# Kernel tuning notes

Hardware: AMD Instinct MI355X
Metric: run time of the kernel (lower is better)

The kernel has to match this reference:

```python
import jax, jax.numpy as jnp
import numpy as np

B, N, H = 16, 1024, 1024


def setup_inputs() -> dict:
    key = jax.random.key(0)
    ks = jax.random.split(key, 12)
    inv = 1.0 / np.sqrt(H)
    inp = {
        "x": jax.random.normal(ks[0], (B, N, H), jnp.float32),
        "atom_graph": jax.random.normal(ks[1], (B, N, N), jnp.float32),
        "variable_graph": jax.random.normal(ks[2], (B, N, N), jnp.float32),
        "Wq": jax.random.uniform(ks[3], (H, H), jnp.float32, -inv, inv),
        "bq": jax.random.uniform(ks[4], (H,), jnp.float32, -inv, inv),
        "Wk": jax.random.uniform(ks[5], (H, H), jnp.float32, -inv, inv),
        "bk": jax.random.uniform(ks[6], (H,), jnp.float32, -inv, inv),
        "Wv": jax.random.uniform(ks[7], (H, H), jnp.float32, -inv, inv),
        "bv": jax.random.uniform(ks[8], (H,), jnp.float32, -inv, inv),
        "predicate_pos": jax.random.randint(ks[9], (B, N), 0, 2, jnp.int32),
        "variable_tags": jax.random.randint(ks[10], (B, N), 0, 4, jnp.int32),
    }
    return inp


def _path_pool(h, predicate_pos):
    # h: [B,N,H]; predicate_pos: [B,N] in {0,1}
    b, n, d = h.shape
    i = jnp.arange(n)
    # pos[i-2] (value irrelevant for i<2, those branches handled explicitly)
    pp2 = jnp.pad(predicate_pos, ((0, 0), (2, 0)))[:, :n]  # [B,N]
    # window [s, e): i==0 -> [0,2); i==1 -> [0,3); pos[i-2]==1 -> [i,i+2); else [i-1,i+2)
    s = jnp.where(i < 2, 0, jnp.where(pp2 == 1, i, i - 1))  # [B,N]
    e = jnp.where(i == 0, 2, jnp.where(i == 1, 3, i + 2))    # [N]
    e = jnp.minimum(e, n)
    e = jnp.broadcast_to(e, (b, n))
    # prefix sums along node dim with a leading zero row -> windowed means via gather
    cs = jnp.concatenate([jnp.zeros((b, 1, d), h.dtype), jnp.cumsum(h, axis=1)], axis=1)  # [B,N+1,H]
    win_sum = (jnp.take_along_axis(cs, e[:, :, None], axis=1)
               - jnp.take_along_axis(cs, s[:, :, None], axis=1))  # [B,N,H]
    means = win_sum / (e - s)[:, :, None].astype(h.dtype)
    mask = (predicate_pos == 1).astype(h.dtype)  # [B,N]
    item = (means * mask[:, :, None]).sum(axis=1) / mask.sum(axis=1)[:, None]  # [B,H]
    return jnp.broadcast_to(item[:, None, :], (b, n, d))


def reference(x, atom_graph, variable_graph, Wq, bq, Wk, bk, Wv, bv,
              predicate_pos, variable_tags):
    scale = x.shape[-1] ** (-0.5)
    q = (x @ Wq.T + bq) * scale
    k = x @ Wk.T + bk
    v = x @ Wv.T + bv
    att = jnp.einsum("bnh,bmh->bnm", q, k) + atom_graph + variable_graph
    att = jax.nn.softmax(att, axis=-1)  # dropout is identity in eval
    h = jnp.einsum("bnm,bmh->bnh", att, v)
    return _path_pool(h, predicate_pos)
```

## Files before the change

kernel.cpp:

```cpp
#include <hip/hip_runtime.h>
#include <hip/hip_bf16.h>

#define BATCH 16
#define SEQ   1024
#define DIM   1024

typedef __attribute__((ext_vector_type(8))) short bf16x8;
typedef __attribute__((ext_vector_type(4))) float f32x4;
typedef __attribute__((ext_vector_type(4))) unsigned short us4;

__device__ __forceinline__ float bfu2f(unsigned short u) {
  union { unsigned int i; float f; } c; c.i = ((unsigned int)u) << 16; return c.f;
}
__device__ __forceinline__ unsigned short f2bfu(float f) {
  union { float f; unsigned int i; } c; c.f = f;
  return (unsigned short)((c.i + 0x7FFFu + ((c.i >> 16) & 1u)) >> 16);
}
__device__ __forceinline__ void async16(void* lds, const void* g) {
  __builtin_amdgcn_global_load_lds(
      (const __attribute__((address_space(1))) unsigned int*)g,
      (__attribute__((address_space(3))) unsigned int*)lds, 16, 0, 0);
}

__global__ void cast_xw_kernel(const float* __restrict__ x, const float* __restrict__ Wv,
                               unsigned short* __restrict__ xb,
                               unsigned short* __restrict__ Wvb, int x4) {
  int i = blockIdx.x * blockDim.x + threadIdx.x;
  const float* in; unsigned short* out; int j;
  if (i < x4) { in = x; out = xb; j = i; }
  else { in = Wv; out = Wvb; j = i - x4; }
  f32x4 v = ((const f32x4*)in)[j];
  us4 o;
  o[0] = f2bfu(v[0]); o[1] = f2bfu(v[1]); o[2] = f2bfu(v[2]); o[3] = f2bfu(v[3]);
  ((us4*)out)[j] = o;
}

__global__ void castT_kernel(const float* __restrict__ Wq, const float* __restrict__ Wk,
                             unsigned short* __restrict__ WqT,
                             unsigned short* __restrict__ WkT) {
  const float* in = (blockIdx.z == 0) ? Wq : Wk;
  unsigned short* out = (blockIdx.z == 0) ? WqT : WkT;
  __shared__ float t[64][65];
  const int h0 = blockIdx.x * 64, i0 = blockIdx.y * 64;
  const int tid = threadIdx.x;
  const int sub = tid >> 4, c4 = tid & 15;
#pragma unroll
  for (int p = 0; p < 4; ++p) {
    const int row = p * 16 + sub;
    f32x4 v = *(const f32x4*)(in + (size_t)(h0 + row) * DIM + i0 + c4 * 4);
    t[row][c4 * 4 + 0] = v[0]; t[row][c4 * 4 + 1] = v[1];
    t[row][c4 * 4 + 2] = v[2]; t[row][c4 * 4 + 3] = v[3];
  }
  __syncthreads();
#pragma unroll
  for (int p = 0; p < 4; ++p) {
    const int orow = p * 16 + sub;
    us4 o;
    o[0] = f2bfu(t[c4 * 4 + 0][orow]);
    o[1] = f2bfu(t[c4 * 4 + 1][orow]);
    o[2] = f2bfu(t[c4 * 4 + 2][orow]);
    o[3] = f2bfu(t[c4 * 4 + 3][orow]);
    *(us4*)(out + (size_t)(i0 + orow) * DIM + h0 + c4 * 4) = o;
  }
}

__global__ void t12_kernel(const unsigned short* __restrict__ WqT,
                           const unsigned short* __restrict__ WkT,
                           const float* __restrict__ bq, const float* __restrict__ bk,
                           float* __restrict__ t1, float* __restrict__ t2) {
  const int y = blockIdx.y;
  const unsigned short* Wt = y ? WkT : WqT;
  const float* vec = y ? bq : bk;
  float* tout = y ? t2 : t1;
  const int wave = threadIdx.x >> 6, lane = threadIdx.x & 63;
  const int i = blockIdx.x * 4 + wave;
  const us4* wr = (const us4*)(Wt + (size_t)i * DIM);
  float s = 0.f;
#pragma unroll
  for (int t = 0; t < 4; ++t) {
    us4 w4 = wr[lane + 64 * t];
    f32x4 b4 = *(const f32x4*)(vec + (lane + 64 * t) * 4);
    s += bfu2f(w4[0]) * b4[0] + bfu2f(w4[1]) * b4[1] +
         bfu2f(w4[2]) * b4[2] + bfu2f(w4[3]) * b4[3];
  }
#pragma unroll
  for (int o = 32; o; o >>= 1) s += __shfl_down(s, o);
  if (lane == 0) tout[i] = s;
}

__global__ void ac_kernel(const unsigned short* __restrict__ xb,
                          const float* __restrict__ t1, const float* __restrict__ t2,
                          const float* __restrict__ bq, const float* __restrict__ bk,
                          float* __restrict__ a, float* __restrict__ c) {
  const float scale = 0.03125f;
  const int tid = threadIdx.x;
  const int wave = tid >> 6, lane = tid & 63;
  float dp = 0.f;
  for (int i = tid; i < DIM; i += 256) dp += bq[i] * bk[i];
#pragma unroll
  for (int o = 32; o; o >>= 1) dp += __shfl_down(dp, o);
  __shared__ float dred[4];
  if ((tid & 63) == 0) dred[tid >> 6] = dp;
  __syncthreads();
  const float d = dred[0] + dred[1] + dred[2] + dred[3];
  float t1r[16], t2r[16];
#pragma unroll
  for (int t = 0; t < 4; ++t) {
    f32x4 v1 = *(const f32x4*)(t1 + (lane + 64 * t) * 4);
    f32x4 v2 = *(const f32x4*)(t2 + (lane + 64 * t) * 4);
#pragma unroll
    for (int j = 0; j < 4; ++j) { t1r[t * 4 + j] = v1[j]; t2r[t * 4 + j] = v2[j]; }
  }
  for (int rr = 0; rr < 16; ++rr) {
    const int row = blockIdx.x * 64 + wave * 16 + rr;
    const us4* xr = (const us4*)(xb + (size_t)row * DIM);
    float sa = 0.f, sc = 0.f;
#pragma unroll
    for (int t = 0; t < 4; ++t) {
      us4 v = xr[lane + 64 * t];
#pragma unroll
      for (int j = 0; j < 4; ++j) {
        const float f = bfu2f(v[j]);
        sa += f * t1r[t * 4 + j];
        sc += f * t2r[t * 4 + j];
      }
    }
#pragma unroll
    for (int o = 32; o; o >>= 1) { sa += __shfl_down(sa, o); sc += __shfl_down(sc, o); }
    if (lane == 0) {
      a[row] = scale * (sa + d);
      c[row] = scale * sc;
    }
  }
}

__global__ void pathw_kernel(const int* __restrict__ pos, float* __restrict__ w,
                             float* __restrict__ denom, float* __restrict__ zbias) {
  const int b = blockIdx.x;
  __shared__ int ps[SEQ];
  __shared__ int mcnt;
  const int tid = threadIdx.x;
  if (tid == 0) mcnt = 0;
  __syncthreads();
  if (b == 0)
    for (int i = tid; i < DIM; i += 256) zbias[i] = 0.f;
  for (int i = tid; i < SEQ; i += 256) {
    ps[i] = pos[b * SEQ + i];
    denom[b * SEQ + i] = 0.f;
  }
  __syncthreads();
  int c = 0;
  for (int i = tid; i < SEQ; i += 256) c += ps[i];
  for (int o = 32; o; o >>= 1) c += __shfl_down(c, o);
  if ((tid & 63) == 0) atomicAdd(&mcnt, c);
  __syncthreads();
  const float invM = 1.0f / (float)mcnt;
  for (int j = tid; j < SEQ; j += 256) {
    float a = 0.f;
#pragma unroll
    for (int di = -1; di <= 1; ++di) {
      int i = j + di;
      if (i < 0 || i >= SEQ) continue;
      if (!ps[i]) continue;
      int s, e;
      if (i < 2) { s = 0; e = (i == 0) ? 2 : 3; }
      else { s = (ps[i - 2] == 1) ? i : (i - 1); e = i + 2; if (e > SEQ) e = SEQ; }
      if (s <= j && j < e) a += 1.0f / (float)(e - s);
    }
    w[b * SEQ + j] = a * invM;
  }
}

__global__ void proj_gemm(const unsigned short* __restrict__ A,
                          const unsigned short* __restrict__ W,
                          const float* __restrict__ bias, float alpha,
                          unsigned short* __restrict__ C, int M, int N, int K)
{
  __shared__ __align__(16) char smem[32768];
  float* Sl = (float*)smem;
  const int tid = threadIdx.x;
  const int wave = tid >> 6, lane = tid & 63;
  const int lr = lane & 15, lg = lane >> 4;
  const int wr = wave >> 1, wc = wave & 1;
  const int flat = blockIdx.x + gridDim.x * blockIdx.y;
  const int q8 = (gridDim.x * gridDim.y) >> 3;
  const int t = (flat & 7) * q8 + (flat >> 3);
  const int m0 = (t / gridDim.y) * 128;
  const int n0 = (t % gridDim.y) * 128;
  const int off0 = tid * 16, off1 = 4096 + tid * 16;
  const int r0 = off0 >> 6, ke0 = (off0 >> 1) & 31;
  const int r1 = off1 >> 6, ke1 = (off1 >> 1) & 31;
  f32x4 acc[4][4] = {};

  auto stage = [&](char* base, int kk) {
    async16(base + off0, A + (size_t)(m0 + r0) * K + kk + ke0);
    async16(base + off1, A + (size_t)(m0 + r1) * K + kk + ke1);
    async16(base + 8192 + off0, W + (size_t)(n0 + r0) * K + kk + ke0);
    async16(base + 8192 + off1, W + (size_t)(n0 + r1) * K + kk + ke1);
  };
  auto compute = [&](const char* base) {
    bf16x8 af[4], bfv[4];
#pragma unroll
    for (int i = 0; i < 4; ++i) {
      af[i]  = *(const bf16x8*)(base + ((wr * 64 + i * 16 + lr) << 6) + (lg << 4));
      bfv[i] = *(const bf16x8*)(base + 8192 + ((wc * 64 + i * 16 + lr) << 6) + (lg << 4));
    }
#pragma unroll
    for (int i = 0; i < 4; ++i)
#pragma unroll
      for (int j = 0; j < 4; ++j)
        acc[i][j] = __builtin_amdgcn_mfma_f32_16x16x32_bf16(af[i], bfv[j], acc[i][j], 0, 0, 0);
  };

  const int nt = K >> 5;
  stage(smem, 0);
  __syncthreads();
  int cur = 0;
  for (int k = 0; k < nt - 1; ++k) {
    stage(smem + ((cur ^ 1) << 14), (k + 1) << 5);
    compute(smem + (cur << 14));
    __syncthreads();
    cur ^= 1;
  }
  compute(smem + (cur << 14));
#pragma unroll
  for (int p = 0; p < 4; ++p) {
    __syncthreads();
    if (wr == (p >> 1)) {
      const int ibase = (p & 1) * 2;
#pragma unroll
      for (int ii = 0; ii < 2; ++ii) {
        const int i = ibase + ii;
#pragma unroll
        for (int j = 0; j < 4; ++j)
#pragma unroll
          for (int r = 0; r < 4; ++r)
            Sl[(ii * 16 + lg * 4 + r) * 132 + wc * 64 + j * 16 + lr] = acc[i][j][r];
      }
    }
    __syncthreads();
#pragma unroll
    for (int it = 0; it < 4; ++it) {
      const int v = tid + it * 256;
      const int lrow = v >> 5, c4 = v & 31;
      const int grow = m0 + p * 32 + lrow;
      const int col = n0 + c4 * 4;
      const f32x4 s4 = *(const f32x4*)(&Sl[lrow * 132 + c4 * 4]);
      const f32x4 b4 = *(const f32x4*)(bias + col);
      us4 o;
      o[0] = f2bfu((s4[0] + b4[0]) * alpha);
      o[1] = f2bfu((s4[1] + b4[1]) * alpha);
      o[2] = f2bfu((s4[2] + b4[2]) * alpha);
      o[3] = f2bfu((s4[3] + b4[3]) * alpha);
      *(us4*)(C + (size_t)grow * N + col) = o;
    }
  }
}

__global__ void qk_exp_kernel(const unsigned short* __restrict__ z,
                              const unsigned short* __restrict__ xb,
                              const float* __restrict__ ag,
                              const float* __restrict__ vg,
                              const float* __restrict__ av,
                              const float* __restrict__ cv,
                              unsigned short* __restrict__ E,
                              float* __restrict__ denom)
{
  __shared__ __align__(16) char smem[33792];
  unsigned short* Slb = (unsigned short*)smem;
  const int flat = blockIdx.x + 8 * blockIdx.y + 64 * blockIdx.z;
  const int t = (flat & 7) * 128 + (flat >> 3);
  const int b = t >> 6;
  const int m0 = (t & 7) * 128;
  const int n0 = ((t >> 3) & 7) * 128;
  const unsigned short* Aq = z + ((size_t)b << 20);
  const unsigned short* Bk = xb + ((size_t)b << 20);
  const int tid = threadIdx.x;
  const int wave = tid >> 6, lane = tid & 63;
  const int lr = lane & 15, lg = lane >> 4;
  const int wr = wave >> 1, wc = wave & 1;
  const int off0 = tid * 16, off1 = 4096 + tid * 16;
  const int r0 = off0 >> 6, ke0 = (off0 >> 1) & 31;
  const int r1 = off1 >> 6, ke1 = (off1 >> 1) & 31;
  f32x4 acc[4][4] = {};

  auto stage = [&](char* base, int kk) {
    async16(base + off0, Aq + (size_t)(m0 + r0) * DIM + kk + ke0);
    async16(base + off1, Aq + (size_t)(m0 + r1) * DIM + kk + ke1);
    async16(base + 8192 + off0, Bk + (size_t)(n0 + r0) * DIM + kk + ke0);
    async16(base + 8192 + off1, Bk + (size_t)(n0 + r1) * DIM + kk + ke1);
  };
  auto compute = [&](const char* base) {
    bf16x8 af[4], bfv[4];
#pragma unroll
    for (int i = 0; i < 4; ++i) {
      af[i]  = *(const bf16x8*)(base + ((wr * 64 + i * 16 + lr) << 6) + (lg << 4));
      bfv[i] = *(const bf16x8*)(base + 8192 + ((wc * 64 + i * 16 + lr) << 6) + (lg << 4));
    }
#pragma unroll
    for (int i = 0; i < 4; ++i)
#pragma unroll
      for (int j = 0; j < 4; ++j)
        acc[i][j] = __builtin_amdgcn_mfma_f32_16x16x32_bf16(af[i], bfv[j], acc[i][j], 0, 0, 0);
  };

  stage(smem, 0);
  __syncthreads();
  int cur = 0;
  for (int k = 0; k < 31; ++k) {
    stage(smem + ((cur ^ 1) << 14), (k + 1) << 5);
    compute(smem + (cur << 14));
    __syncthreads();
    cur ^= 1;
  }
  compute(smem + (cur << 14));
  __syncthreads();
#pragma unroll
  for (int i = 0; i < 4; ++i)
#pragma unroll
    for (int j = 0; j < 4; ++j)
#pragma unroll
      for (int r = 0; r < 4; ++r)
        Slb[(wr * 64 + i * 16 + lg * 4 + r) * 132 + wc * 64 + j * 16 + lr] =
            f2bfu(acc[i][j][r]);
  __syncthreads();
  const float* agb = ag + ((size_t)b << 20);
  const float* vgb = vg + ((size_t)b << 20);
  unsigned short* Eb = E + ((size_t)b << 20);
  float* dnb = denom + b * SEQ;
  const float* avb = av + b * SEQ;
  const float* cvb = cv + b * SEQ;
#pragma unroll
  for (int bt = 0; bt < 4; ++bt) {
    f32x4 a4[4], g4[4];
    int lrow[4];
    size_t basev[4];
#pragma unroll
    for (int q = 0; q < 4; ++q) {
      const int v = tid + (bt * 4 + q) * 256;
      lrow[q] = v >> 5;
      const int c4 = v & 31;
      basev[q] = (size_t)(m0 + lrow[q]) * SEQ + n0 + c4 * 4;
      a4[q] = *(const f32x4*)(agb + basev[q]);
      g4[q] = *(const f32x4*)(vgb + basev[q]);
    }
#pragma unroll
    for (int q = 0; q < 4; ++q) {
      const int v = tid + (bt * 4 + q) * 256;
      const int c4 = v & 31;
      const f32x4 c4v = *(const f32x4*)(cvb + n0 + c4 * 4);
      const float arow = avb[m0 + lrow[q]];
      const us4 sv = *(const us4*)(&Slb[lrow[q] * 132 + c4 * 4]);
      const float e0 = __expf(bfu2f(sv[0]) + a4[q][0] + g4[q][0] + arow + c4v[0]);
      const float e1 = __expf(bfu2f(sv[1]) + a4[q][1] + g4[q][1] + arow + c4v[1]);
      const float e2 = __expf(bfu2f(sv[2]) + a4[q][2] + g4[q][2] + arow + c4v[2]);
      const float e3 = __expf(bfu2f(sv[3]) + a4[q][3] + g4[q][3] + arow + c4v[3]);
      us4 o;
      o[0] = f2bfu(e0); o[1] = f2bfu(e1); o[2] = f2bfu(e2); o[3] = f2bfu(e3);
      *(us4*)(Eb + basev[q]) = o;
      float rs = e0 + e1 + e2 + e3;
#pragma unroll
      for (int o2 = 16; o2; o2 >>= 1) rs += __shfl_down(rs, o2, 32);
      if ((tid & 31) == 0) atomicAdd(&dnb[m0 + lrow[q]], rs);
    }
  }
}

__global__ void wcol_kernel(const unsigned short* __restrict__ Mt,
                            const float* __restrict__ wv,
                            const float* __restrict__ dv,
                            float* __restrict__ part) {
  const int nc = blockIdx.x;
  const int b = blockIdx.y;
  const int tid = threadIdx.x;
  __shared__ float c[64];
  if (tid < 64) {
    const int n = nc * 64 + tid;
    float cvw = wv[b * SEQ + n];
    if (dv) cvw /= dv[b * SEQ + n];
    c[tid] = cvw;
  }
  __syncthreads();
  const unsigned short* p = Mt + ((size_t)b << 20) + ((size_t)(nc * 64) << 10) + tid * 4;
  f32x4 acc = {0.f, 0.f, 0.f, 0.f};
#pragma unroll 8
  for (int n = 0; n < 64; ++n) {
    const us4 v = *(const us4*)(p + ((size_t)n << 10));
    const float cn = c[n];
    acc[0] += cn * bfu2f(v[0]); acc[1] += cn * bfu2f(v[1]);
    acc[2] += cn * bfu2f(v[2]); acc[3] += cn * bfu2f(v[3]);
  }
  *(f32x4*)(part + (size_t)((b * 16 + nc) << 10) + tid * 4) = acc;
}

__global__ void wred_kernel(const float* __restrict__ part, float* __restrict__ vec,
                            float* __restrict__ su) {
  const int b = blockIdx.x;
  const int tid = threadIdx.x;
  f32x4 s = {0.f, 0.f, 0.f, 0.f};
#pragma unroll
  for (int nc = 0; nc < 16; ++nc) {
    const f32x4 v = *(const f32x4*)(part + (size_t)((b * 16 + nc) << 10) + tid * 4);
    s[0] += v[0]; s[1] += v[1]; s[2] += v[2]; s[3] += v[3];
  }
  *(f32x4*)(vec + b * SEQ + tid * 4) = s;
  if (su) {
    float ts = s[0] + s[1] + s[2] + s[3];
#pragma unroll
    for (int o = 32; o; o >>= 1) ts += __shfl_down(ts, o);
    __shared__ float red[4];
    if ((tid & 63) == 0) red[tid >> 6] = ts;
    __syncthreads();
    if (tid == 0) su[b] = red[0] + red[1] + red[2] + red[3];
  }
}

__global__ void item_kernel(const float* __restrict__ y, const float* __restrict__ su,
                            const unsigned short* __restrict__ Wvb,
                            const float* __restrict__ bv, float* __restrict__ item) {
  const int b = blockIdx.x;
  const int hblk = blockIdx.y;
  __shared__ float ys[DIM];
  const int tid = threadIdx.x;
  for (int i = tid; i < DIM; i += 256) ys[i] = y[b * DIM + i];
  __syncthreads();
  const float sub = su[b];
  const int wave = tid >> 6, lane = tid & 63;
  const int h = hblk * 4 + wave;
  const us4* wrow = (const us4*)(Wvb + (size_t)h * DIM);
  float acc = 0.f;
#pragma unroll
  for (int t = 0; t < 4; ++t) {
    us4 v = wrow[t * 64 + lane];
    const int d0 = (t * 64 + lane) * 4;
    acc += ys[d0] * bfu2f(v[0]) + ys[d0 + 1] * bfu2f(v[1]) +
           ys[d0 + 2] * bfu2f(v[2]) + ys[d0 + 3] * bfu2f(v[3]);
  }
  for (int o = 32; o; o >>= 1) acc += __shfl_down(acc, o);
  if (lane == 0) item[b * DIM + h] = acc + sub * bv[h];
}

__global__ void bcast_kernel(const float* __restrict__ item, float* __restrict__ out) {
  const int b = blockIdx.y;
  const int n = blockIdx.x;
  const f32x4* src = (const f32x4*)(item + b * DIM);
  f32x4* dst = (f32x4*)(out + (((size_t)b * SEQ + n) << 10));
  dst[threadIdx.x] = src[threadIdx.x];
}

extern "C" void kernel_launch(void* const* d_in, const int* in_sizes, int n_in,
                              void* d_out, int out_size, void* d_ws, size_t ws_size,
                              hipStream_t stream) {
  const float* x    = (const float*)d_in[0];
  const float* ag   = (const float*)d_in[1];
  const float* vgr  = (const float*)d_in[2];
  const float* Wq   = (const float*)d_in[3];
  const float* bq   = (const float*)d_in[4];
  const float* Wk   = (const float*)d_in[5];
  const float* bk   = (const float*)d_in[6];
  const float* Wv   = (const float*)d_in[7];
  const float* bv   = (const float*)d_in[8];
  const int*   pos  = (const int*)d_in[9];
  float* out = (float*)d_out;

  char* ws = (char*)d_ws;
  size_t off = 0;
  auto alloc = [&](size_t bytes) { void* p = ws + off; off += (bytes + 255) & ~(size_t)255; return p; };
  const size_t BNH = (size_t)BATCH * SEQ * DIM;
  unsigned short* xb   = (unsigned short*)alloc(BNH * 2);
  unsigned short* zb   = (unsigned short*)alloc(BNH * 2);
  unsigned short* E    = (unsigned short*)alloc(BNH * 2);
  unsigned short* WqT  = (unsigned short*)alloc((size_t)DIM * DIM * 2);
  unsigned short* WkT  = (unsigned short*)alloc((size_t)DIM * DIM * 2);
  unsigned short* Wvb  = (unsigned short*)alloc((size_t)DIM * DIM * 2);
  unsigned short* Hb   = (unsigned short*)alloc((size_t)DIM * DIM * 2);
  float* w     = (float*)alloc((size_t)BATCH * SEQ * 4);
  float* denom = (float*)alloc((size_t)BATCH * SEQ * 4);
  float* u     = (float*)alloc((size_t)BATCH * SEQ * 4);
  float* av    = (float*)alloc((size_t)BATCH * SEQ * 4);
  float* cvv   = (float*)alloc((size_t)BATCH * SEQ * 4);
  float* t1    = (float*)alloc((size_t)DIM * 4);
  float* t2    = (float*)alloc((size_t)DIM * 4);
  float* zbias = (float*)alloc((size_t)DIM * 4);
  float* y     = (float*)alloc((size_t)BATCH * DIM * 4);
  float* su    = (float*)alloc((size_t)BATCH * 4);
  float* item  = (float*)alloc((size_t)BATCH * DIM * 4);
  float* part  = (float*)alloc((size_t)BATCH * 16 * SEQ * 4);

  const float scale = 0.03125f;
  const int x4 = (int)(BNH / 4);

  cast_xw_kernel<<<(x4 + DIM * DIM / 4) / 256, 256, 0, stream>>>(x, Wv, xb, Wvb, x4);
  castT_kernel<<<dim3(16, 16, 2), 256, 0, stream>>>(Wq, Wk, WqT, WkT);

  pathw_kernel<<<BATCH, 256, 0, stream>>>(pos, w, denom, zbias);

  t12_kernel<<<dim3(256, 2), 256, 0, stream>>>(WqT, WkT, bq, bk, t1, t2);
  ac_kernel<<<256, 256, 0, stream>>>(xb, t1, t2, bq, bk, av, cvv);

  proj_gemm<<<dim3(8, 8), 256, 0, stream>>>(WkT, WqT, zbias, scale, Hb, DIM, DIM, DIM);

  proj_gemm<<<dim3(128, 8), 256, 0, stream>>>(xb, Hb, zbias, 1.0f, zb,
                                              BATCH * SEQ, DIM, DIM);

  qk_exp_kernel<<<dim3(8, 8, BATCH), 256, 0, stream>>>(zb, xb, ag, vgr, av, cvv, E, denom);

  wcol_kernel<<<dim3(16, BATCH), 256, 0, stream>>>(E, w, denom, part);
  wred_kernel<<<BATCH, 256, 0, stream>>>(part, u, su);

  wcol_kernel<<<dim3(16, BATCH), 256, 0, stream>>>(xb, u, nullptr, part);
  wred_kernel<<<BATCH, 256, 0, stream>>>(part, y, nullptr);

  item_kernel<<<dim3(BATCH, 256), 256, 0, stream>>>(y, su, Wvb, bv, item);

  bcast_kernel<<<dim3(SEQ, BATCH), 256, 0, stream>>>(item, out);
}
```

Baseline: 216.9 us.

## Split QK GEMM and exp epilogue into separate kernels with row-wise denominators

The fused QK^T GEMM plus exp epilogue is split into two kernels. The GEMM now writes bf16 scores to E. A separate row-oriented kernel then adds both graph biases, exponentiates in place, and writes each row's sum directly, which removes the atomics and the need to zero the denominators. The cost is an extra round trip of the bf16 score matrix through global memory and one more launch, in exchange for a simpler GEMM epilogue and contiguous row-wise access to the fp32 graph tensors.

```diff
diff --git a/kernel.cpp b/kernel.cpp
--- a/kernel.cpp
+++ b/kernel.cpp
@@ -135,7 +135,7 @@
 }
 
 __global__ void pathw_kernel(const int* __restrict__ pos, float* __restrict__ w,
-                             float* __restrict__ denom, float* __restrict__ zbias) {
+                             float* __restrict__ zbias) {
   const int b = blockIdx.x;
   __shared__ int ps[SEQ];
   __shared__ int mcnt;
@@ -144,10 +144,7 @@
   __syncthreads();
   if (b == 0)
     for (int i = tid; i < DIM; i += 256) zbias[i] = 0.f;
-  for (int i = tid; i < SEQ; i += 256) {
-    ps[i] = pos[b * SEQ + i];
-    denom[b * SEQ + i] = 0.f;
-  }
+  for (int i = tid; i < SEQ; i += 256) ps[i] = pos[b * SEQ + i];
   __syncthreads();
   int c = 0;
   for (int i = tid; i < SEQ; i += 256) c += ps[i];
@@ -257,14 +254,9 @@
   }
 }
 
-__global__ void qk_exp_kernel(const unsigned short* __restrict__ z,
-                              const unsigned short* __restrict__ xb,
-                              const float* __restrict__ ag,
-                              const float* __restrict__ vg,
-                              const float* __restrict__ av,
-                              const float* __restrict__ cv,
-                              unsigned short* __restrict__ E,
-                              float* __restrict__ denom)
+__global__ void sgemm_kernel(const unsigned short* __restrict__ z,
+                             const unsigned short* __restrict__ xb,
+                             unsigned short* __restrict__ S)
 {
   __shared__ __align__(16) char smem[33792];
   unsigned short* Slb = (unsigned short*)smem;
@@ -324,45 +316,59 @@
         Slb[(wr * 64 + i * 16 + lg * 4 + r) * 132 + wc * 64 + j * 16 + lr] =
             f2bfu(acc[i][j][r]);
   __syncthreads();
+  unsigned short* Sb = S + ((size_t)b << 20);
+#pragma unroll
+  for (int it = 0; it < 16; ++it) {
+    const int v = tid + it * 256;
+    const int lrow = v >> 5, c4 = v & 31;
+    *(us4*)(Sb + (size_t)(m0 + lrow) * SEQ + n0 + c4 * 4) =
+        *(const us4*)(&Slb[lrow * 132 + c4 * 4]);
+  }
+}
+
+__global__ void exp_kernel(unsigned short* __restrict__ SE,
+                           const float* __restrict__ ag, const float* __restrict__ vg,
+                           const float* __restrict__ av, const float* __restrict__ cv,
+                           float* __restrict__ denom)
+{
+  const int b = blockIdx.y;
+  const int wave = threadIdx.x >> 6, lane = threadIdx.x & 63;
+  const int r0 = blockIdx.x * 8 + wave * 2;
   const float* agb = ag + ((size_t)b << 20);
   const float* vgb = vg + ((size_t)b << 20);
-  unsigned short* Eb = E + ((size_t)b << 20);
-  float* dnb = denom + b * SEQ;
-  const float* avb = av + b * SEQ;
   const float* cvb = cv + b * SEQ;
-#pragma unroll
-  for (int bt = 0; bt < 4; ++bt) {
-    f32x4 a4[4], g4[4];
-    int lrow[4];
-    size_t basev[4];
-#pragma unroll
-    for (int q = 0; q < 4; ++q) {
-      const int v = tid + (bt * 4 + q) * 256;
-      lrow[q] = v >> 5;
-      const int c4 = v & 31;
-      basev[q] = (size_t)(m0 + lrow[q]) * SEQ + n0 + c4 * 4;
-      a4[q] = *(const f32x4*)(agb + basev[q]);
-      g4[q] = *(const f32x4*)(vgb + basev[q]);
-    }
-#pragma unroll
-    for (int q = 0; q < 4; ++q) {
-      const int v = tid + (bt * 4 + q) * 256;
-      const int c4 = v & 31;
-      const f32x4 c4v = *(const f32x4*)(cvb + n0 + c4 * 4);
-      const float arow = avb[m0 + lrow[q]];
-      const us4 sv = *(const us4*)(&Slb[lrow[q] * 132 + c4 * 4]);
-      const float e0 = __expf(bfu2f(sv[0]) + a4[q][0] + g4[q][0] + arow + c4v[0]);
-      const float e1 = __expf(bfu2f(sv[1]) + a4[q][1] + g4[q][1] + arow + c4v[1]);
-      const float e2 = __expf(bfu2f(sv[2]) + a4[q][2] + g4[q][2] + arow + c4v[2]);
-      const float e3 = __expf(bfu2f(sv[3]) + a4[q][3] + g4[q][3] + arow + c4v[3]);
+  unsigned short* Eb = SE + ((size_t)b << 20);
+#pragma unroll
+  for (int r = 0; r < 2; ++r) {
+    const int row = r0 + r;
+    const float arow = av[b * SEQ + row];
+    us4 sv[4]; f32x4 a4[4], g4[4], cq[4];
+#pragma unroll
+    for (int qi = 0; qi < 4; ++qi) {
+      const int col = (lane + 64 * qi) * 4;
+      const size_t base = (size_t)row * SEQ + col;
+      sv[qi] = *(const us4*)(Eb + base);
+      a4[qi] = *(const f32x4*)(agb + base);
+      g4[qi] = *(const f32x4*)(vgb + base);
+      cq[qi] = *(const f32x4*)(cvb + col);
+    }
+    float rs = 0.f;
+#pragma unroll
+    for (int qi = 0; qi < 4; ++qi) {
+      const int col = (lane + 64 * qi) * 4;
+      const size_t base = (size_t)row * SEQ + col;
+      const float e0 = __expf(bfu2f(sv[qi][0]) + a4[qi][0] + g4[qi][0] + arow + cq[qi][0]);
+      const float e1 = __expf(bfu2f(sv[qi][1]) + a4[qi][1] + g4[qi][1] + arow + cq[qi][1]);
+      const float e2 = __expf(bfu2f(sv[qi][2]) + a4[qi][2] + g4[qi][2] + arow + cq[qi][2]);
+      const float e3 = __expf(bfu2f(sv[qi][3]) + a4[qi][3] + g4[qi][3] + arow + cq[qi][3]);
       us4 o;
       o[0] = f2bfu(e0); o[1] = f2bfu(e1); o[2] = f2bfu(e2); o[3] = f2bfu(e3);
-      *(us4*)(Eb + basev[q]) = o;
-      float rs = e0 + e1 + e2 + e3;
-#pragma unroll
-      for (int o2 = 16; o2; o2 >>= 1) rs += __shfl_down(rs, o2, 32);
-      if ((tid & 31) == 0) atomicAdd(&dnb[m0 + lrow[q]], rs);
-    }
+      *(us4*)(Eb + base) = o;
+      rs += e0 + e1 + e2 + e3;
+    }
+#pragma unroll
+    for (int o2 = 32; o2; o2 >>= 1) rs += __shfl_down(rs, o2);
+    if (lane == 0) denom[b * SEQ + row] = rs;
   }
 }
 
@@ -493,7 +499,7 @@
   cast_xw_kernel<<<(x4 + DIM * DIM / 4) / 256, 256, 0, stream>>>(x, Wv, xb, Wvb, x4);
   castT_kernel<<<dim3(16, 16, 2), 256, 0, stream>>>(Wq, Wk, WqT, WkT);
 
-  pathw_kernel<<<BATCH, 256, 0, stream>>>(pos, w, denom, zbias);
+  pathw_kernel<<<BATCH, 256, 0, stream>>>(pos, w, zbias);
 
   t12_kernel<<<dim3(256, 2), 256, 0, stream>>>(WqT, WkT, bq, bk, t1, t2);
   ac_kernel<<<256, 256, 0, stream>>>(xb, t1, t2, bq, bk, av, cvv);
@@ -503,7 +509,9 @@
   proj_gemm<<<dim3(128, 8), 256, 0, stream>>>(xb, Hb, zbias, 1.0f, zb,
                                               BATCH * SEQ, DIM, DIM);
 
-  qk_exp_kernel<<<dim3(8, 8, BATCH), 256, 0, stream>>>(zb, xb, ag, vgr, av, cvv, E, denom);
+  sgemm_kernel<<<dim3(8, 8, BATCH), 256, 0, stream>>>(zb, xb, E);
+
+  exp_kernel<<<dim3(128, BATCH), 256, 0, stream>>>(E, ag, vgr, av, cvv, denom);
 
   wcol_kernel<<<dim3(16, BATCH), 256, 0, stream>>>(E, w, denom, part);
   wred_kernel<<<BATCH, 256, 0, stream>>>(part, u, su);
```

After: 223.5 us. 3.1% more time.
